# Kernel optimization log

Hardware: AMD Instinct MI355X
Metric: run time of the kernel (lower is better)

The kernel has to match this reference:

```python
import jax, jax.numpy as jnp
import numpy as np

EPS = 1e-5
D_MODEL, D_INNER, D_STATE, DT_RANK, K = 2048, 4096, 16, 128, 4

def setup_inputs() -> dict:
    key = jax.random.key(0)
    ks = jax.random.split(key, 13)
    B = 128
    s = lambda k, shape, sc=0.02: jax.random.normal(k, shape, jnp.float32) * sc
    return {
        "hidden_states": jax.random.normal(ks[0], (B, 1, D_MODEL), jnp.float32),
        "conv_state": jax.random.normal(ks[1], (B, D_INNER, K - 1), jnp.float32),
        "ssm_state": jax.random.normal(ks[2], (B, D_INNER, D_STATE), jnp.float32),
        "norm_w": jnp.ones((D_MODEL,), jnp.float32),
        "in_proj_w": s(ks[3], (2 * D_INNER, D_MODEL)),           # no bias (HF Mamba default)
        "conv_w": s(ks[4], (D_INNER, K), 0.1),                    # depthwise conv kernel
        "conv_b": s(ks[5], (D_INNER,), 0.1),
        "x_proj_w": s(ks[6], (DT_RANK + 2 * D_STATE, D_INNER)),
        "dt_proj_w": s(ks[7], (D_INNER, DT_RANK)),
        "dt_proj_b": s(ks[8], (D_INNER,), 0.1),
        "A_log": jnp.log(jnp.broadcast_to(jnp.arange(1, D_STATE + 1, dtype=jnp.float32), (D_INNER, D_STATE))),
        "D": jnp.ones((D_INNER,), jnp.float32),
        "out_proj_w": s(ks[9], (D_MODEL, D_INNER)),               # no bias
    }

def reference(hidden_states, conv_state, ssm_state, norm_w, in_proj_w, conv_w, conv_b,
              x_proj_w, dt_proj_w, dt_proj_b, A_log, D, out_proj_w):
    x = hidden_states[:, 0, :]                                   # (B, d_model)
    # RMSNorm (pre-norm)
    normed = x * jax.lax.rsqrt(jnp.mean(x * x, axis=-1, keepdims=True) + EPS) * norm_w
    # in_proj -> gate z and conv branch xc
    xz = normed @ in_proj_w.T                                    # (B, 2*d_inner)
    xc, z = jnp.split(xz, 2, axis=-1)
    # depthwise causal conv, single-step with rolling cache
    conv_in = jnp.concatenate([conv_state, xc[:, :, None]], axis=-1)  # (B, d_inner, K)
    new_conv_state = conv_in[:, :, 1:]
    xact = jax.nn.silu(jnp.sum(conv_in * conv_w[None], axis=-1) + conv_b)  # (B, d_inner)
    # input-dependent SSM params
    proj = xact @ x_proj_w.T                                     # (B, dt_rank + 2*d_state)
    dt_raw = proj[:, :DT_RANK]
    Bmat = proj[:, DT_RANK:DT_RANK + D_STATE]                    # (B, d_state)
    Cmat = proj[:, DT_RANK + D_STATE:]                           # (B, d_state)
    dt = jax.nn.softplus(dt_raw @ dt_proj_w.T + dt_proj_b)       # (B, d_inner)
    A = -jnp.exp(A_log)                                          # (d_inner, d_state)
    dA = jnp.exp(dt[:, :, None] * A[None])                       # (B, d_inner, d_state)
    dB = dt[:, :, None] * Bmat[:, None, :]
    new_ssm_state = ssm_state * dA + dB * xact[:, :, None]
    y = jnp.sum(new_ssm_state * Cmat[:, None, :], axis=-1) + D * xact
    y = y * jax.nn.silu(z)
    out = y @ out_proj_w.T                                       # (B, d_model)
    output = out[:, None, :] + hidden_states                     # residual add
    return output, new_conv_state, new_ssm_state
```

## Files before the change

kernel.cpp:

```cpp
#include <hip/hip_runtime.h>

typedef __attribute__((ext_vector_type(8))) short bf16x8;
typedef __attribute__((ext_vector_type(4))) float f32x4;
typedef __attribute__((ext_vector_type(8))) unsigned short u16x8;
typedef __attribute__((ext_vector_type(4))) unsigned short u16x4;

#define DM 2048
#define DI 4096
#define BATCH 128

__device__ __forceinline__ unsigned short f2bf(float f) {
  union { float f; unsigned u; } v; v.f = f;
  unsigned r = v.u + 0x7FFFu + ((v.u >> 16) & 1u);
  return (unsigned short)(r >> 16);
}
__device__ __forceinline__ float bf2f(unsigned short u) {
  union { unsigned u; float f; } v; v.u = (unsigned)u << 16; return v.f;
}
__device__ __forceinline__ float sigm(float x) { return 1.f / (1.f + __expf(-x)); }

constexpr int BK = 64;
constexpr int LDT = BK + 8;

template<int BN, bool ABF>
__device__ __forceinline__ void gemm128(const void* Ag, int lda, const float* Bg, int ldb,
                                        int n0, int k0, int k1, unsigned short* lds,
                                        f32x4* acc) {
  constexpr int NF = BN / 32;
  constexpr int BUF = (128 + BN) * LDT;
  const int tid = threadIdx.x, lane = tid & 63, wave = tid >> 6;
  const int wm = wave >> 1, wn = wave & 1, llo = lane & 15, lhi = lane >> 4;

  u16x8 ar[ABF ? 4 : 1];
  f32x4 arf[ABF ? 1 : 8];
  f32x4 br[BN / 16];

  auto ldregs = [&](int kb) {
    if constexpr (ABF) {
#pragma unroll
      for (int i = 0; i < 4; ++i) {
        int idx = tid + i * 256, r = idx >> 3, c = (idx & 7) * 8;
        ar[i] = *(const u16x8*)&((const unsigned short*)Ag)[(long)r * lda + kb + c];
      }
    } else {
#pragma unroll
      for (int i = 0; i < 8; ++i) {
        int idx = tid + i * 256, r = idx >> 4, c = (idx & 15) * 4;
        arf[i] = *(const f32x4*)&((const float*)Ag)[(long)r * lda + kb + c];
      }
    }
#pragma unroll
    for (int i = 0; i < BN / 16; ++i) {
      int idx = tid + i * 256, r = idx >> 4, c = (idx & 15) * 4;
      br[i] = *(const f32x4*)&Bg[(long)(n0 + r) * ldb + kb + c];
    }
  };

  auto stlds = [&](int buf) {
    unsigned short* As = lds + buf * BUF;
    unsigned short* Bs = As + 128 * LDT;
    if constexpr (ABF) {
#pragma unroll
      for (int i = 0; i < 4; ++i) {
        int idx = tid + i * 256, r = idx >> 3, c = (idx & 7) * 8;
        *(u16x8*)&As[r * LDT + c] = ar[i];
      }
    } else {
#pragma unroll
      for (int i = 0; i < 8; ++i) {
        int idx = tid + i * 256, r = idx >> 4, c = (idx & 15) * 4;
        u16x4 o; o[0] = f2bf(arf[i][0]); o[1] = f2bf(arf[i][1]);
        o[2] = f2bf(arf[i][2]); o[3] = f2bf(arf[i][3]);
        *(u16x4*)&As[r * LDT + c] = o;
      }
    }
#pragma unroll
    for (int i = 0; i < BN / 16; ++i) {
      int idx = tid + i * 256, r = idx >> 4, c = (idx & 15) * 4;
      u16x4 o; o[0] = f2bf(br[i][0]); o[1] = f2bf(br[i][1]);
      o[2] = f2bf(br[i][2]); o[3] = f2bf(br[i][3]);
      *(u16x4*)&Bs[r * LDT + c] = o;
    }
  };

  ldregs(k0);
  stlds(0);
  __syncthreads();
  const int nt = (k1 - k0) / BK;
  int cur = 0;
  for (int t = 0; t < nt; ++t) {
    if (t + 1 < nt) ldregs(k0 + (t + 1) * BK);
    const unsigned short* As = lds + cur * BUF;
    const unsigned short* Bs = As + 128 * LDT;
#pragma unroll
    for (int kk = 0; kk < BK; kk += 32) {
      int kr = kk + lhi * 8;
      bf16x8 af[4], bf[NF];
#pragma unroll
      for (int mi = 0; mi < 4; ++mi)
        af[mi] = *(const bf16x8*)&As[(wm * 64 + mi * 16 + llo) * LDT + kr];
#pragma unroll
      for (int ni = 0; ni < NF; ++ni)
        bf[ni] = *(const bf16x8*)&Bs[(wn * 16 * NF + ni * 16 + llo) * LDT + kr];
#pragma unroll
      for (int mi = 0; mi < 4; ++mi)
#pragma unroll
        for (int ni = 0; ni < NF; ++ni)
          acc[mi * NF + ni] =
              __builtin_amdgcn_mfma_f32_16x16x32_bf16(af[mi], bf[ni], acc[mi * NF + ni], 0, 0, 0);
    }
    if (t + 1 < nt) stlds(cur ^ 1);
    __syncthreads();
    cur ^= 1;
  }
}

__global__ __launch_bounds__(256) void k0_prep(const float* __restrict__ hs,
                                               float* __restrict__ outp,
                                               float* __restrict__ xz,
                                               float* __restrict__ proj) {
  int t = blockIdx.x * 256 + threadIdx.x;
  f32x4 z = {};
  *(f32x4*)&xz[t * 4] = z;
  if (t < 65536) *(f32x4*)&outp[t * 4] = *(const f32x4*)&hs[t * 4];
  if (t < 5120) *(f32x4*)&proj[t * 4] = z;
}

__global__ __launch_bounds__(256) void k1_rmsnorm(const float* __restrict__ hs,
                                                  const float* __restrict__ nw,
                                                  unsigned short* __restrict__ normed) {
  int b = blockIdx.x, tid = threadIdx.x;
  const float* xr = hs + (long)b * DM;
  f32x4 v0 = *(const f32x4*)&xr[tid * 4];
  f32x4 v1 = *(const f32x4*)&xr[(tid + 256) * 4];
  float ss = v0[0]*v0[0] + v0[1]*v0[1] + v0[2]*v0[2] + v0[3]*v0[3]
           + v1[0]*v1[0] + v1[1]*v1[1] + v1[2]*v1[2] + v1[3]*v1[3];
  for (int off = 32; off; off >>= 1) ss += __shfl_xor(ss, off);
  __shared__ float red[4];
  if ((tid & 63) == 0) red[tid >> 6] = ss;
  __syncthreads();
  ss = red[0] + red[1] + red[2] + red[3];
  float rstd = rsqrtf(ss * (1.f / DM) + 1e-5f);
  f32x4 w0 = *(const f32x4*)&nw[tid * 4];
  f32x4 w1 = *(const f32x4*)&nw[(tid + 256) * 4];
  u16x4 o0, o1;
#pragma unroll
  for (int j = 0; j < 4; ++j) {
    o0[j] = f2bf(v0[j] * rstd * w0[j]);
    o1[j] = f2bf(v1[j] * rstd * w1[j]);
  }
  *(u16x4*)&normed[(long)b * DM + tid * 4] = o0;
  *(u16x4*)&normed[(long)b * DM + (tid + 256) * 4] = o1;
}

__global__ __launch_bounds__(256) void k2_inproj(const unsigned short* __restrict__ normed,
                                                 const float* __restrict__ W,
                                                 float* __restrict__ xz) {
  __shared__ unsigned short lds[2 * (128 + 64) * LDT];
  f32x4 acc[8] = {};
  int bn = blockIdx.x, sk = blockIdx.y;
  gemm128<64, true>(normed, DM, W, DM, bn * 64, sk * 512, sk * 512 + 512, lds, acc);
  int tid = threadIdx.x, lane = tid & 63, wave = tid >> 6, wm = wave >> 1, wn = wave & 1;
  int llo = lane & 15, lhi = lane >> 4;
#pragma unroll
  for (int mi = 0; mi < 4; ++mi)
#pragma unroll
    for (int ni = 0; ni < 2; ++ni)
#pragma unroll
      for (int r = 0; r < 4; ++r) {
        int b = wm * 64 + mi * 16 + lhi * 4 + r;
        int n = bn * 64 + wn * 32 + ni * 16 + llo;
        atomicAdd(&xz[(long)b * 8192 + n], acc[mi * 2 + ni][r]);
      }
}

__global__ __launch_bounds__(256) void e2_conv(const float* __restrict__ xz,
                                               const float* __restrict__ conv_state,
                                               const float* __restrict__ conv_w,
                                               const float* __restrict__ conv_b,
                                               float* __restrict__ out_ncs,
                                               float* __restrict__ xact_f,
                                               unsigned short* __restrict__ xact_b,
                                               unsigned short* __restrict__ szb) {
  int p = blockIdx.x * 256 + threadIdx.x;
  int b = p >> 12, n = p & 4095;
  float xc = xz[(long)b * 8192 + n];
  float z  = xz[(long)b * 8192 + DI + n];
  const float* cs = conv_state + (long)p * 3;
  float c0 = cs[0], c1 = cs[1], c2 = cs[2];
  f32x4 cw = *(const f32x4*)&conv_w[n * 4];
  float xs = c0 * cw[0] + c1 * cw[1] + c2 * cw[2] + xc * cw[3] + conv_b[n];
  float xa = xs * sigm(xs);
  float* ncs = out_ncs + (long)p * 3;
  ncs[0] = c1; ncs[1] = c2; ncs[2] = xc;
  xact_f[p] = xa;
  xact_b[p] = f2bf(xa);
  szb[p] = f2bf(z * sigm(z));
}

__global__ __launch_bounds__(256) void k3_xproj(const unsigned short* __restrict__ xact_b,
                                                const float* __restrict__ XW,
                                                float* __restrict__ proj) {
  __shared__ unsigned short lds[2 * (128 + 32) * LDT];
  f32x4 acc[4] = {};
  int bn = blockIdx.x, kc = blockIdx.y;
  gemm128<32, true>(xact_b, DI, XW, DI, bn * 32, kc * 256, kc * 256 + 256, lds, acc);
  int tid = threadIdx.x, lane = tid & 63, wave = tid >> 6, wm = wave >> 1, wn = wave & 1;
  int llo = lane & 15, lhi = lane >> 4;
  int n = bn * 32 + wn * 16 + llo;
#pragma unroll
  for (int mi = 0; mi < 4; ++mi)
#pragma unroll
    for (int r = 0; r < 4; ++r) {
      int b = wm * 64 + mi * 16 + lhi * 4 + r;
      atomicAdd(&proj[b * 160 + n], acc[mi][r]);
    }
}

__global__ __launch_bounds__(256) void k4a_dt(const float* __restrict__ proj,
                                              const float* __restrict__ DW,
                                              const float* __restrict__ dtb,
                                              float* __restrict__ dt_f) {
  __shared__ unsigned short lds[2 * (128 + 64) * LDT];
  f32x4 acc[8] = {};
  int bn = blockIdx.x;
  gemm128<64, false>(proj, 160, DW, 128, bn * 64, 0, 128, lds, acc);
  int tid = threadIdx.x, lane = tid & 63, wave = tid >> 6, wm = wave >> 1, wn = wave & 1;
  int llo = lane & 15, lhi = lane >> 4;
#pragma unroll
  for (int mi = 0; mi < 4; ++mi)
#pragma unroll
    for (int ni = 0; ni < 2; ++ni) {
      int n = bn * 64 + wn * 32 + ni * 16 + llo;
      float db = dtb[n];
#pragma unroll
      for (int r = 0; r < 4; ++r) {
        int b = wm * 64 + mi * 16 + lhi * 4 + r;
        float v = acc[mi * 2 + ni][r] + db;
        dt_f[(long)b * DI + n] = (v > 20.f) ? v : log1pf(__expf(v));
      }
    }
}

__global__ __launch_bounds__(256) void k4b_ssm(const float* __restrict__ dt_f,
                                               const float* __restrict__ proj,
                                               const float* __restrict__ A_log,
                                               const float* __restrict__ Dp,
                                               const float* __restrict__ ssm,
                                               const float* __restrict__ xact_f,
                                               const unsigned short* __restrict__ szb,
                                               float* __restrict__ out_nss,
                                               unsigned short* __restrict__ yz_b) {
  int t = blockIdx.x * 256 + threadIdx.x;
  int s4 = t & 3;
  int p0 = t >> 2;
  const int STRIDE = (2048 * 256) >> 2;
#pragma unroll
  for (int it = 0; it < 4; ++it) {
    int p = p0 + it * STRIDE;
    int b = p >> 12, n = p & 4095;
    float dtv = dt_f[p];
    float xa = xact_f[p];
    f32x4 sv = *(const f32x4*)&ssm[(long)p * 16 + s4 * 4];
    f32x4 Al = *(const f32x4*)&A_log[n * 16 + s4 * 4];
    f32x4 Bv = *(const f32x4*)&proj[b * 160 + 128 + s4 * 4];
    f32x4 Cv = *(const f32x4*)&proj[b * 160 + 144 + s4 * 4];
    f32x4 nv;
    float y = 0.f;
#pragma unroll
    for (int j = 0; j < 4; ++j) {
      float dA = __expf(dtv * (-__expf(Al[j])));
      nv[j] = sv[j] * dA + dtv * Bv[j] * xa;
      y += nv[j] * Cv[j];
    }
    *(f32x4*)&out_nss[(long)p * 16 + s4 * 4] = nv;
    y += __shfl_xor(y, 1);
    y += __shfl_xor(y, 2);
    if (s4 == 0) yz_b[p] = f2bf((y + Dp[n] * xa) * bf2f(szb[p]));
  }
}

__global__ __launch_bounds__(256) void k5_outproj(const unsigned short* __restrict__ yz_b,
                                                  const float* __restrict__ OW,
                                                  float* __restrict__ outp) {
  __shared__ unsigned short lds[2 * (128 + 32) * LDT];
  f32x4 acc[4] = {};
  int bn = blockIdx.x, sk = blockIdx.y;
  gemm128<32, true>(yz_b, DI, OW, DI, bn * 32, sk * 512, sk * 512 + 512, lds, acc);
  int tid = threadIdx.x, lane = tid & 63, wave = tid >> 6, wm = wave >> 1, wn = wave & 1;
  int llo = lane & 15, lhi = lane >> 4;
  int n = bn * 32 + wn * 16 + llo;
#pragma unroll
  for (int mi = 0; mi < 4; ++mi)
#pragma unroll
    for (int r = 0; r < 4; ++r) {
      int b = wm * 64 + mi * 16 + lhi * 4 + r;
      atomicAdd(&outp[(long)b * DM + n], acc[mi][r]);
    }
}

extern "C" void kernel_launch(void* const* d_in, const int* in_sizes, int n_in, void* d_out,
                              int out_size, void* d_ws, size_t ws_size, hipStream_t stream) {
  const float* hs         = (const float*)d_in[0];
  const float* conv_state = (const float*)d_in[1];
  const float* ssm        = (const float*)d_in[2];
  const float* norm_w     = (const float*)d_in[3];
  const float* in_proj_w  = (const float*)d_in[4];
  const float* conv_w     = (const float*)d_in[5];
  const float* conv_b     = (const float*)d_in[6];
  const float* x_proj_w   = (const float*)d_in[7];
  const float* dt_proj_w  = (const float*)d_in[8];
  const float* dt_proj_b  = (const float*)d_in[9];
  const float* A_log      = (const float*)d_in[10];
  const float* Dp         = (const float*)d_in[11];
  const float* out_proj_w = (const float*)d_in[12];

  float* outp    = (float*)d_out;
  float* out_ncs = outp + 262144;
  float* out_nss = outp + 262144 + 1572864;

  char* ws = (char*)d_ws;
  unsigned short* normed = (unsigned short*)(ws);
  float*          dt_f   = (float*)(ws);
  float*          xz     = (float*)(ws + 2097152);
  unsigned short* yz_b   = (unsigned short*)(ws + 2097152);
  float*          xact_f = (float*)(ws + 6291456);
  unsigned short* xact_b = (unsigned short*)(ws + 8388608);
  unsigned short* szb    = (unsigned short*)(ws + 9437184);
  float*          proj   = (float*)(ws + 10485760);

  hipLaunchKernelGGL(k0_prep, dim3(1024), dim3(256), 0, stream, hs, outp, xz, proj);
  hipLaunchKernelGGL(k1_rmsnorm, dim3(128), dim3(256), 0, stream, hs, norm_w, normed);
  hipLaunchKernelGGL(k2_inproj, dim3(128, 4), dim3(256), 0, stream, normed, in_proj_w, xz);
  hipLaunchKernelGGL(e2_conv, dim3(2048), dim3(256), 0, stream, xz, conv_state, conv_w, conv_b,
                     out_ncs, xact_f, xact_b, szb);
  hipLaunchKernelGGL(k3_xproj, dim3(5, 16), dim3(256), 0, stream, xact_b, x_proj_w, proj);
  hipLaunchKernelGGL(k4a_dt, dim3(64), dim3(256), 0, stream, proj, dt_proj_w, dt_proj_b, dt_f);
  hipLaunchKernelGGL(k4b_ssm, dim3(2048), dim3(256), 0, stream, dt_f, proj, A_log, Dp, ssm,
                     xact_f, szb, out_nss, yz_b);
  hipLaunchKernelGGL(k5_outproj, dim3(64, 8), dim3(256), 0, stream, yz_b, out_proj_w, outp);
}
```

Baseline: 85.16 us.

## Deepen GEMM prefetch, fuse rmsnorm into prep, split x_proj and dt grids finer

The shared GEMM helper now keeps two register stage sets, so global loads for tile t+2 are issued while tile t is computed, and the loop is unrolled over the two LDS buffers. The RMSNorm kernel is merged into the zero-fill/copy prep kernel to save one launch. x_proj now splits K into 128-wide chunks over twice as many blocks, and the dt GEMM uses 32-wide N tiles over 128 blocks, both to raise parallelism on a small problem. The cost is more live registers, possibly lower occupancy, and twice as many atomics into proj.

```diff
diff --git a/kernel.cpp b/kernel.cpp
--- a/kernel.cpp
+++ b/kernel.cpp
@@ -21,6 +21,66 @@
 
 constexpr int BK = 64;
 constexpr int LDT = BK + 8;
+
+#define LDREGS(AR, ARF, BR, kb_) do {                                                     \
+    int kb = (kb_);                                                                       \
+    if constexpr (ABF) {                                                                  \
+      _Pragma("unroll") for (int i = 0; i < 4; ++i) {                                     \
+        int idx = tid + i * 256, r = idx >> 3, c = (idx & 7) * 8;                         \
+        AR[i] = *(const u16x8*)&((const unsigned short*)Ag)[(long)r * lda + kb + c];      \
+      }                                                                                   \
+    } else {                                                                              \
+      _Pragma("unroll") for (int i = 0; i < 8; ++i) {                                     \
+        int idx = tid + i * 256, r = idx >> 4, c = (idx & 15) * 4;                        \
+        ARF[i] = *(const f32x4*)&((const float*)Ag)[(long)r * lda + kb + c];              \
+      }                                                                                   \
+    }                                                                                     \
+    _Pragma("unroll") for (int i = 0; i < BN / 16; ++i) {                                 \
+      int idx = tid + i * 256, r = idx >> 4, c = (idx & 15) * 4;                          \
+      BR[i] = *(const f32x4*)&Bg[(long)(n0 + r) * ldb + kb + c];                          \
+    }                                                                                     \
+  } while (0)
+
+#define STLDS(AR, ARF, BR, buf_) do {                                                     \
+    unsigned short* As_ = lds + (buf_) * BUF;                                             \
+    unsigned short* Bs_ = As_ + 128 * LDT;                                                \
+    if constexpr (ABF) {                                                                  \
+      _Pragma("unroll") for (int i = 0; i < 4; ++i) {                                     \
+        int idx = tid + i * 256, r = idx >> 3, c = (idx & 7) * 8;                         \
+        *(u16x8*)&As_[r * LDT + c] = AR[i];                                               \
+      }                                                                                   \
+    } else {                                                                              \
+      _Pragma("unroll") for (int i = 0; i < 8; ++i) {                                     \
+        int idx = tid + i * 256, r = idx >> 4, c = (idx & 15) * 4;                        \
+        u16x4 o; o[0] = f2bf(ARF[i][0]); o[1] = f2bf(ARF[i][1]);                          \
+        o[2] = f2bf(ARF[i][2]); o[3] = f2bf(ARF[i][3]);                                   \
+        *(u16x4*)&As_[r * LDT + c] = o;                                                   \
+      }                                                                                   \
+    }                                                                                     \
+    _Pragma("unroll") for (int i = 0; i < BN / 16; ++i) {                                 \
+      int idx = tid + i * 256, r = idx >> 4, c = (idx & 15) * 4;                          \
+      u16x4 o; o[0] = f2bf(BR[i][0]); o[1] = f2bf(BR[i][1]);                              \
+      o[2] = f2bf(BR[i][2]); o[3] = f2bf(BR[i][3]);                                       \
+      *(u16x4*)&Bs_[r * LDT + c] = o;                                                     \
+    }                                                                                     \
+  } while (0)
+
+#define COMPUTE(buf_) do {                                                                \
+    const unsigned short* As_ = lds + (buf_) * BUF;                                       \
+    const unsigned short* Bs_ = As_ + 128 * LDT;                                          \
+    _Pragma("unroll") for (int kk = 0; kk < BK; kk += 32) {                               \
+      int kr = kk + lhi * 8;                                                              \
+      bf16x8 af[4], bfr[NF];                                                              \
+      _Pragma("unroll") for (int mi = 0; mi < 4; ++mi)                                    \
+        af[mi] = *(const bf16x8*)&As_[(wm * 64 + mi * 16 + llo) * LDT + kr];              \
+      _Pragma("unroll") for (int ni = 0; ni < NF; ++ni)                                   \
+        bfr[ni] = *(const bf16x8*)&Bs_[(wn * 16 * NF + ni * 16 + llo) * LDT + kr];        \
+      _Pragma("unroll") for (int mi = 0; mi < 4; ++mi)                                    \
+        _Pragma("unroll") for (int ni = 0; ni < NF; ++ni)                                 \
+          acc[mi * NF + ni] = __builtin_amdgcn_mfma_f32_16x16x32_bf16(                    \
+              af[mi], bfr[ni], acc[mi * NF + ni], 0, 0, 0);                               \
+    }                                                                                     \
+  } while (0)
 
 template<int BN, bool ABF>
 __device__ __forceinline__ void gemm128(const void* Ag, int lda, const float* Bg, int ldb,
@@ -31,126 +91,66 @@
   const int tid = threadIdx.x, lane = tid & 63, wave = tid >> 6;
   const int wm = wave >> 1, wn = wave & 1, llo = lane & 15, lhi = lane >> 4;
 
-  u16x8 ar[ABF ? 4 : 1];
-  f32x4 arf[ABF ? 1 : 8];
-  f32x4 br[BN / 16];
-
-  auto ldregs = [&](int kb) {
-    if constexpr (ABF) {
-#pragma unroll
-      for (int i = 0; i < 4; ++i) {
-        int idx = tid + i * 256, r = idx >> 3, c = (idx & 7) * 8;
-        ar[i] = *(const u16x8*)&((const unsigned short*)Ag)[(long)r * lda + kb + c];
-      }
-    } else {
-#pragma unroll
-      for (int i = 0; i < 8; ++i) {
-        int idx = tid + i * 256, r = idx >> 4, c = (idx & 15) * 4;
-        arf[i] = *(const f32x4*)&((const float*)Ag)[(long)r * lda + kb + c];
-      }
-    }
-#pragma unroll
-    for (int i = 0; i < BN / 16; ++i) {
-      int idx = tid + i * 256, r = idx >> 4, c = (idx & 15) * 4;
-      br[i] = *(const f32x4*)&Bg[(long)(n0 + r) * ldb + kb + c];
-    }
-  };
-
-  auto stlds = [&](int buf) {
-    unsigned short* As = lds + buf * BUF;
-    unsigned short* Bs = As + 128 * LDT;
-    if constexpr (ABF) {
-#pragma unroll
-      for (int i = 0; i < 4; ++i) {
-        int idx = tid + i * 256, r = idx >> 3, c = (idx & 7) * 8;
-        *(u16x8*)&As[r * LDT + c] = ar[i];
-      }
-    } else {
-#pragma unroll
-      for (int i = 0; i < 8; ++i) {
-        int idx = tid + i * 256, r = idx >> 4, c = (idx & 15) * 4;
-        u16x4 o; o[0] = f2bf(arf[i][0]); o[1] = f2bf(arf[i][1]);
-        o[2] = f2bf(arf[i][2]); o[3] = f2bf(arf[i][3]);
-        *(u16x4*)&As[r * LDT + c] = o;
-      }
-    }
-#pragma unroll
-    for (int i = 0; i < BN / 16; ++i) {
-      int idx = tid + i * 256, r = idx >> 4, c = (idx & 15) * 4;
-      u16x4 o; o[0] = f2bf(br[i][0]); o[1] = f2bf(br[i][1]);
-      o[2] = f2bf(br[i][2]); o[3] = f2bf(br[i][3]);
-      *(u16x4*)&Bs[r * LDT + c] = o;
-    }
-  };
-
-  ldregs(k0);
-  stlds(0);
+  u16x8 ar0[ABF ? 4 : 1], ar1[ABF ? 4 : 1];
+  f32x4 arf0[ABF ? 1 : 8], arf1[ABF ? 1 : 8];
+  f32x4 br0[BN / 16], br1[BN / 16];
+
+  const int nt = (k1 - k0) / BK;
+  LDREGS(ar0, arf0, br0, k0);
+  LDREGS(ar1, arf1, br1, k0 + BK);
+  STLDS(ar0, arf0, br0, 0);
   __syncthreads();
-  const int nt = (k1 - k0) / BK;
-  int cur = 0;
-  for (int t = 0; t < nt; ++t) {
-    if (t + 1 < nt) ldregs(k0 + (t + 1) * BK);
-    const unsigned short* As = lds + cur * BUF;
-    const unsigned short* Bs = As + 128 * LDT;
-#pragma unroll
-    for (int kk = 0; kk < BK; kk += 32) {
-      int kr = kk + lhi * 8;
-      bf16x8 af[4], bf[NF];
-#pragma unroll
-      for (int mi = 0; mi < 4; ++mi)
-        af[mi] = *(const bf16x8*)&As[(wm * 64 + mi * 16 + llo) * LDT + kr];
-#pragma unroll
-      for (int ni = 0; ni < NF; ++ni)
-        bf[ni] = *(const bf16x8*)&Bs[(wn * 16 * NF + ni * 16 + llo) * LDT + kr];
-#pragma unroll
-      for (int mi = 0; mi < 4; ++mi)
-#pragma unroll
-        for (int ni = 0; ni < NF; ++ni)
-          acc[mi * NF + ni] =
-              __builtin_amdgcn_mfma_f32_16x16x32_bf16(af[mi], bf[ni], acc[mi * NF + ni], 0, 0, 0);
-    }
-    if (t + 1 < nt) stlds(cur ^ 1);
+  int t = 0;
+  while (true) {
+    if (t + 2 < nt) LDREGS(ar0, arf0, br0, k0 + (t + 2) * BK);
+    COMPUTE(0);
+    if (t + 1 < nt) STLDS(ar1, arf1, br1, 1);
     __syncthreads();
-    cur ^= 1;
+    if (++t == nt) break;
+    if (t + 2 < nt) LDREGS(ar1, arf1, br1, k0 + (t + 2) * BK);
+    COMPUTE(1);
+    if (t + 1 < nt) STLDS(ar0, arf0, br0, 0);
+    __syncthreads();
+    if (++t == nt) break;
   }
 }
 
-__global__ __launch_bounds__(256) void k0_prep(const float* __restrict__ hs,
-                                               float* __restrict__ outp,
-                                               float* __restrict__ xz,
-                                               float* __restrict__ proj) {
-  int t = blockIdx.x * 256 + threadIdx.x;
+__global__ __launch_bounds__(256) void k01_prep(const float* __restrict__ hs,
+                                                const float* __restrict__ nw,
+                                                unsigned short* __restrict__ normed,
+                                                float* __restrict__ outp,
+                                                float* __restrict__ xz,
+                                                float* __restrict__ proj) {
+  int blk = blockIdx.x, tid = threadIdx.x;
+  int t = blk * 256 + tid;
   f32x4 z = {};
   *(f32x4*)&xz[t * 4] = z;
   if (t < 65536) *(f32x4*)&outp[t * 4] = *(const f32x4*)&hs[t * 4];
   if (t < 5120) *(f32x4*)&proj[t * 4] = z;
-}
-
-__global__ __launch_bounds__(256) void k1_rmsnorm(const float* __restrict__ hs,
-                                                  const float* __restrict__ nw,
-                                                  unsigned short* __restrict__ normed) {
-  int b = blockIdx.x, tid = threadIdx.x;
-  const float* xr = hs + (long)b * DM;
-  f32x4 v0 = *(const f32x4*)&xr[tid * 4];
-  f32x4 v1 = *(const f32x4*)&xr[(tid + 256) * 4];
-  float ss = v0[0]*v0[0] + v0[1]*v0[1] + v0[2]*v0[2] + v0[3]*v0[3]
-           + v1[0]*v1[0] + v1[1]*v1[1] + v1[2]*v1[2] + v1[3]*v1[3];
-  for (int off = 32; off; off >>= 1) ss += __shfl_xor(ss, off);
-  __shared__ float red[4];
-  if ((tid & 63) == 0) red[tid >> 6] = ss;
-  __syncthreads();
-  ss = red[0] + red[1] + red[2] + red[3];
-  float rstd = rsqrtf(ss * (1.f / DM) + 1e-5f);
-  f32x4 w0 = *(const f32x4*)&nw[tid * 4];
-  f32x4 w1 = *(const f32x4*)&nw[(tid + 256) * 4];
-  u16x4 o0, o1;
-#pragma unroll
-  for (int j = 0; j < 4; ++j) {
-    o0[j] = f2bf(v0[j] * rstd * w0[j]);
-    o1[j] = f2bf(v1[j] * rstd * w1[j]);
+  if (blk < 128) {
+    int b = blk;
+    const float* xr = hs + (long)b * DM;
+    f32x4 v0 = *(const f32x4*)&xr[tid * 4];
+    f32x4 v1 = *(const f32x4*)&xr[(tid + 256) * 4];
+    float ss = v0[0]*v0[0] + v0[1]*v0[1] + v0[2]*v0[2] + v0[3]*v0[3]
+             + v1[0]*v1[0] + v1[1]*v1[1] + v1[2]*v1[2] + v1[3]*v1[3];
+    for (int off = 32; off; off >>= 1) ss += __shfl_xor(ss, off);
+    __shared__ float red[4];
+    if ((tid & 63) == 0) red[tid >> 6] = ss;
+    __syncthreads();
+    ss = red[0] + red[1] + red[2] + red[3];
+    float rstd = rsqrtf(ss * (1.f / DM) + 1e-5f);
+    f32x4 w0 = *(const f32x4*)&nw[tid * 4];
+    f32x4 w1 = *(const f32x4*)&nw[(tid + 256) * 4];
+    u16x4 o0, o1;
+#pragma unroll
+    for (int j = 0; j < 4; ++j) {
+      o0[j] = f2bf(v0[j] * rstd * w0[j]);
+      o1[j] = f2bf(v1[j] * rstd * w1[j]);
+    }
+    *(u16x4*)&normed[(long)b * DM + tid * 4] = o0;
+    *(u16x4*)&normed[(long)b * DM + (tid + 256) * 4] = o1;
   }
-  *(u16x4*)&normed[(long)b * DM + tid * 4] = o0;
-  *(u16x4*)&normed[(long)b * DM + (tid + 256) * 4] = o1;
 }
 
 __global__ __launch_bounds__(256) void k2_inproj(const unsigned short* __restrict__ normed,
@@ -204,7 +204,7 @@
   __shared__ unsigned short lds[2 * (128 + 32) * LDT];
   f32x4 acc[4] = {};
   int bn = blockIdx.x, kc = blockIdx.y;
-  gemm128<32, true>(xact_b, DI, XW, DI, bn * 32, kc * 256, kc * 256 + 256, lds, acc);
+  gemm128<32, true>(xact_b, DI, XW, DI, bn * 32, kc * 128, kc * 128 + 128, lds, acc);
   int tid = threadIdx.x, lane = tid & 63, wave = tid >> 6, wm = wave >> 1, wn = wave & 1;
   int llo = lane & 15, lhi = lane >> 4;
   int n = bn * 32 + wn * 16 + llo;
@@ -221,24 +221,21 @@
                                               const float* __restrict__ DW,
                                               const float* __restrict__ dtb,
                                               float* __restrict__ dt_f) {
-  __shared__ unsigned short lds[2 * (128 + 64) * LDT];
-  f32x4 acc[8] = {};
+  __shared__ unsigned short lds[2 * (128 + 32) * LDT];
+  f32x4 acc[4] = {};
   int bn = blockIdx.x;
-  gemm128<64, false>(proj, 160, DW, 128, bn * 64, 0, 128, lds, acc);
+  gemm128<32, false>(proj, 160, DW, 128, bn * 32, 0, 128, lds, acc);
   int tid = threadIdx.x, lane = tid & 63, wave = tid >> 6, wm = wave >> 1, wn = wave & 1;
   int llo = lane & 15, lhi = lane >> 4;
+  int n = bn * 32 + wn * 16 + llo;
+  float db = dtb[n];
 #pragma unroll
   for (int mi = 0; mi < 4; ++mi)
 #pragma unroll
-    for (int ni = 0; ni < 2; ++ni) {
-      int n = bn * 64 + wn * 32 + ni * 16 + llo;
-      float db = dtb[n];
-#pragma unroll
-      for (int r = 0; r < 4; ++r) {
-        int b = wm * 64 + mi * 16 + lhi * 4 + r;
-        float v = acc[mi * 2 + ni][r] + db;
-        dt_f[(long)b * DI + n] = (v > 20.f) ? v : log1pf(__expf(v));
-      }
+    for (int r = 0; r < 4; ++r) {
+      int b = wm * 64 + mi * 16 + lhi * 4 + r;
+      float v = acc[mi][r] + db;
+      dt_f[(long)b * DI + n] = (v > 20.f) ? v : log1pf(__expf(v));
     }
 }
 
@@ -329,13 +326,12 @@
   unsigned short* szb    = (unsigned short*)(ws + 9437184);
   float*          proj   = (float*)(ws + 10485760);
 
-  hipLaunchKernelGGL(k0_prep, dim3(1024), dim3(256), 0, stream, hs, outp, xz, proj);
-  hipLaunchKernelGGL(k1_rmsnorm, dim3(128), dim3(256), 0, stream, hs, norm_w, normed);
+  hipLaunchKernelGGL(k01_prep, dim3(1024), dim3(256), 0, stream, hs, norm_w, normed, outp, xz, proj);
   hipLaunchKernelGGL(k2_inproj, dim3(128, 4), dim3(256), 0, stream, normed, in_proj_w, xz);
   hipLaunchKernelGGL(e2_conv, dim3(2048), dim3(256), 0, stream, xz, conv_state, conv_w, conv_b,
                      out_ncs, xact_f, xact_b, szb);
-  hipLaunchKernelGGL(k3_xproj, dim3(5, 16), dim3(256), 0, stream, xact_b, x_proj_w, proj);
-  hipLaunchKernelGGL(k4a_dt, dim3(64), dim3(256), 0, stream, proj, dt_proj_w, dt_proj_b, dt_f);
+  hipLaunchKernelGGL(k3_xproj, dim3(5, 32), dim3(256), 0, stream, xact_b, x_proj_w, proj);
+  hipLaunchKernelGGL(k4a_dt, dim3(128), dim3(256), 0, stream, proj, dt_proj_w, dt_proj_b, dt_f);
   hipLaunchKernelGGL(k4b_ssm, dim3(2048), dim3(256), 0, stream, dt_f, proj, A_log, Dp, ssm,
                      xact_f, szb, out_nss, yz_b);
   hipLaunchKernelGGL(k5_outproj, dim3(64, 8), dim3(256), 0, stream, yz_b, out_proj_w, outp);
```

Measured after the change: 76.76 us. 9.9% less time.
